# Performance work log

Measured on AMD Instinct MI355X. Metric: run time of the kernel, lower is better.

The kernel has to match this reference:

```python
import jax, jax.numpy as jnp
import numpy as np

B, N, H, E = 4, 256, 128, 32

def setup_inputs() -> dict:
    key = jax.random.key(0)
    ks = jax.random.split(key, 7)
    s = 0.05
    return {
        "node_h": jax.random.normal(ks[0], (B, N, H), dtype=jnp.float32),
        "dart_h": jax.random.normal(ks[1], (B, N, N, H), dtype=jnp.float32),
        "edge_x": jax.random.normal(ks[2], (B, N, N, E), dtype=jnp.float32),
        "W1": jax.random.normal(ks[3], (3 * H + E, H), dtype=jnp.float32) * s,
        "b1": jnp.zeros((H,), dtype=jnp.float32),
        "W2": jax.random.normal(ks[4], (H, H), dtype=jnp.float32) * s,
        "b2": jnp.zeros((H,), dtype=jnp.float32),
    }

def reference(node_h, dart_h, edge_x, W1, b1, W2, b2):
    # Split first-layer weight by concat blocks [src | dst | dart_h | edge_x]
    W1s, W1d, W1h, W1e = W1[:H], W1[H:2*H], W1[2*H:3*H], W1[3*H:]
    # Equivalent to mlp(cat([src_expand, dst_expand, dart_h, edge_x])) but
    # computes the small [B,N,H] matmuls before broadcasting to [B,N,N,H].
    pre = (jnp.einsum('bih,hk->bik', node_h, W1s)[:, :, None, :]
           + jnp.einsum('bjh,hk->bjk', node_h, W1d)[:, None, :, :]
           + jnp.einsum('bijh,hk->bijk', dart_h, W1h)
           + jnp.einsum('bije,ek->bijk', edge_x, W1e)
           + b1)
    h = jax.nn.relu(pre)
    return jnp.einsum('bijh,hk->bijk', h, W2) + b2
```

## Files before the change

kernel.cpp:

```cpp
#include <hip/hip_runtime.h>
#include <hip/hip_bf16.h>


typedef __attribute__((ext_vector_type(8))) short bf16x8;
typedef __attribute__((ext_vector_type(4))) short bf16x4;
typedef __attribute__((ext_vector_type(4))) float f32x4;

__device__ __forceinline__ unsigned short f2bf(float f) {
  union { float f; unsigned u; } v; v.f = f;
  unsigned r = v.u + 0x7FFFu + ((v.u >> 16) & 1u);
  return (unsigned short)(r >> 16);
}

__device__ __forceinline__ bf16x4 cvt4(float4 a) {
  bf16x4 r;
  r[0] = (short)f2bf(a.x); r[1] = (short)f2bf(a.y);
  r[2] = (short)f2bf(a.z); r[3] = (short)f2bf(a.w);
  return r;
}

__global__ void prep_kernel(const float* __restrict__ node, const float* __restrict__ W1,
                            const float* __restrict__ b1, const float* __restrict__ W2,
                            float* __restrict__ S, float* __restrict__ D,
                            unsigned short* __restrict__ W1hT, unsigned short* __restrict__ W1eT,
                            unsigned short* __restrict__ W2T) {
  const int t = threadIdx.x;
  if (blockIdx.x < 256) {
    __shared__ float nrow[4 * 128];
    const int bi0 = blockIdx.x * 4;
    if (t < 128)
      reinterpret_cast<float4*>(nrow)[t] = reinterpret_cast<const float4*>(node + bi0 * 128)[t];
    __syncthreads();
    const int kc = t & 127, half = t >> 7;
    float s0 = 0.f, s1 = 0.f, d0 = 0.f, d1 = 0.f;
    for (int h = 0; h < 128; ++h) {
      float ws = W1[h * 128 + kc];
      float wd = W1[(128 + h) * 128 + kc];
      float n0 = nrow[(half * 2) * 128 + h];
      float n1 = nrow[(half * 2 + 1) * 128 + h];
      s0 = fmaf(n0, ws, s0); s1 = fmaf(n1, ws, s1);
      d0 = fmaf(n0, wd, d0); d1 = fmaf(n1, wd, d1);
    }
    const float bv = b1[kc];
    S[(bi0 + half * 2) * 128 + kc] = s0 + bv;
    S[(bi0 + half * 2 + 1) * 128 + kc] = s1 + bv;
    D[(bi0 + half * 2) * 128 + kc] = d0;
    D[(bi0 + half * 2 + 1) * 128 + kc] = d1;
  } else {
    int gid = (blockIdx.x - 256) * 256 + t;
    for (int idx = gid; idx < 16384; idx += 2048)
      W1hT[idx] = f2bf(W1[(256 + (idx & 127)) * 128 + (idx >> 7)]);
    for (int idx = gid; idx < 4096; idx += 2048)
      W1eT[idx] = f2bf(W1[(384 + (idx & 31)) * 128 + (idx >> 5)]);
    for (int idx = gid; idx < 16384; idx += 2048)
      W2T[idx] = f2bf(W2[(idx & 127) * 128 + (idx >> 7)]);
  }
}

#define LDH 140
#define LDE 36

__launch_bounds__(512, 4)
__global__ void fused_kernel(const float* __restrict__ dart, const float* __restrict__ edge,
                             const float* __restrict__ S, const float* __restrict__ D,
                             const unsigned short* __restrict__ W1hT,
                             const unsigned short* __restrict__ W1eT,
                             const unsigned short* __restrict__ W2T,
                             const float* __restrict__ b2, float* __restrict__ out) {
  __shared__ unsigned short sDart[64 * LDH];
  __shared__ unsigned short sEdge[64 * LDE];
  __shared__ unsigned short sH[2][64 * LDH];

  const int tid = threadIdx.x;
  const int lane = tid & 63;
  const int wv = tid >> 6;
  const int g = lane >> 4;
  const int lj = lane & 15;

  const int bi = (blockIdx.x & 7) * 128 + (blockIdx.x >> 3);
  const int b = bi >> 8;
  const size_t m_base = (size_t)bi * 256;

  bf16x8 wh[4], we;
#pragma unroll
  for (int hs = 0; hs < 4; ++hs)
    wh[hs] = *reinterpret_cast<const bf16x8*>(&W1hT[(wv * 16 + lj) * 128 + hs * 32 + g * 8]);
  we = *reinterpret_cast<const bf16x8*>(&W1eT[(wv * 16 + lj) * 32 + g * 8]);

  float sv[4];
#pragma unroll
  for (int r = 0; r < 4; ++r)
    sv[r] = S[bi * 128 + wv * 16 + g * 4 + r];

  const int jh = wv >> 2;
  const int wn = wv & 3;
  float b2v[2][4];
#pragma unroll
  for (int nt = 0; nt < 2; ++nt)
#pragma unroll
    for (int r = 0; r < 4; ++r)
      b2v[nt][r] = b2[wn * 32 + nt * 16 + g * 4 + r];

  const int srow = tid >> 3;
  const int scol = (tid & 3 ? (tid & 7) * 4 : (tid & 7) * 4);

  for (int t = 0; t < 4; ++t) {
    const int j0 = t * 64;

    {
      const float* dsrc = dart + (m_base + j0 + srow) * 128 + scol;
      float4 rd0 = *reinterpret_cast<const float4*>(dsrc);
      float4 rd1 = *reinterpret_cast<const float4*>(dsrc + 32);
      float4 rd2 = *reinterpret_cast<const float4*>(dsrc + 64);
      float4 rd3 = *reinterpret_cast<const float4*>(dsrc + 96);
      float4 re  = *reinterpret_cast<const float4*>(edge + (m_base + j0 + srow) * 32 + scol);
      *reinterpret_cast<bf16x4*>(&sDart[srow * LDH + scol])      = cvt4(rd0);
      *reinterpret_cast<bf16x4*>(&sDart[srow * LDH + scol + 32]) = cvt4(rd1);
      *reinterpret_cast<bf16x4*>(&sDart[srow * LDH + scol + 64]) = cvt4(rd2);
      *reinterpret_cast<bf16x4*>(&sDart[srow * LDH + scol + 96]) = cvt4(rd3);
      *reinterpret_cast<bf16x4*>(&sEdge[srow * LDE + scol])      = cvt4(re);
    }
    __syncthreads();

    f32x4 dv4[4];
    {
      const float* Dp = D + (size_t)(b * 256 + j0 + lj) * 128 + wv * 16 + g * 4;
#pragma unroll
      for (int jt = 0; jt < 4; ++jt)
        dv4[jt] = *reinterpret_cast<const f32x4*>(&Dp[(size_t)(jt * 16) * 128]);
    }

    f32x4 acc1[4];
#pragma unroll
    for (int jt = 0; jt < 4; ++jt) acc1[jt] = (f32x4){0.f, 0.f, 0.f, 0.f};

#pragma unroll
    for (int hs = 0; hs < 4; ++hs) {
#pragma unroll
      for (int jt = 0; jt < 4; ++jt) {
        bf16x8 bd = *reinterpret_cast<const bf16x8*>(&sDart[(jt * 16 + lj) * LDH + hs * 32 + g * 8]);
        acc1[jt] = __builtin_amdgcn_mfma_f32_16x16x32_bf16(wh[hs], bd, acc1[jt], 0, 0, 0);
      }
    }
#pragma unroll
    for (int jt = 0; jt < 4; ++jt) {
      bf16x8 be = *reinterpret_cast<const bf16x8*>(&sEdge[(jt * 16 + lj) * LDE + g * 8]);
      acc1[jt] = __builtin_amdgcn_mfma_f32_16x16x32_bf16(we, be, acc1[jt], 0, 0, 0);
    }

    unsigned short* sHc = sH[t & 1];
#pragma unroll
    for (int jt = 0; jt < 4; ++jt) {
      bf16x4 hp;
#pragma unroll
      for (int r = 0; r < 4; ++r) {
        float x = acc1[jt][r] + sv[r] + dv4[jt][r];
        x = x > 0.f ? x : 0.f;
        hp[r] = (short)f2bf(x);
      }
      *reinterpret_cast<bf16x4*>(&sHc[(jt * 16 + lj) * LDH + wv * 16 + g * 4]) = hp;
    }
    __syncthreads();

    bf16x8 w2f[4][2];
#pragma unroll
    for (int ks = 0; ks < 4; ++ks)
#pragma unroll
      for (int nt = 0; nt < 2; ++nt)
        w2f[ks][nt] = *reinterpret_cast<const bf16x8*>(&W2T[(wn * 32 + nt * 16 + lj) * 128 + ks * 32 + g * 8]);

    f32x4 acc2[2][2];
#pragma unroll
    for (int jt = 0; jt < 2; ++jt)
#pragma unroll
      for (int nt = 0; nt < 2; ++nt) acc2[jt][nt] = (f32x4){0.f, 0.f, 0.f, 0.f};

#pragma unroll
    for (int ks = 0; ks < 4; ++ks) {
#pragma unroll
      for (int jt = 0; jt < 2; ++jt) {
        bf16x8 ah = *reinterpret_cast<const bf16x8*>(&sHc[(jh * 32 + jt * 16 + lj) * LDH + ks * 32 + g * 8]);
        acc2[jt][0] = __builtin_amdgcn_mfma_f32_16x16x32_bf16(w2f[ks][0], ah, acc2[jt][0], 0, 0, 0);
        acc2[jt][1] = __builtin_amdgcn_mfma_f32_16x16x32_bf16(w2f[ks][1], ah, acc2[jt][1], 0, 0, 0);
      }
    }

    {
      float* op = out + (m_base + j0) * 128;
#pragma unroll
      for (int jt = 0; jt < 2; ++jt)
#pragma unroll
        for (int nt = 0; nt < 2; ++nt) {
          float4 v;
          v.x = acc2[jt][nt][0] + b2v[nt][0];
          v.y = acc2[jt][nt][1] + b2v[nt][1];
          v.z = acc2[jt][nt][2] + b2v[nt][2];
          v.w = acc2[jt][nt][3] + b2v[nt][3];
          *reinterpret_cast<float4*>(&op[(size_t)(jh * 32 + jt * 16 + lj) * 128 + wn * 32 + nt * 16 + g * 4]) = v;
        }
    }
  }
}

extern "C" void kernel_launch(void* const* d_in, const int* in_sizes, int n_in,
                              void* d_out, int out_size, void* d_ws, size_t ws_size,
                              hipStream_t stream) {
  const float* node = (const float*)d_in[0];
  const float* dart = (const float*)d_in[1];
  const float* edge = (const float*)d_in[2];
  const float* W1   = (const float*)d_in[3];
  const float* b1   = (const float*)d_in[4];
  const float* W2   = (const float*)d_in[5];
  const float* b2   = (const float*)d_in[6];
  float* out = (float*)d_out;

  float* S  = (float*)d_ws;
  float* D  = S + 131072;
  unsigned short* W1hT = (unsigned short*)(D + 131072);
  unsigned short* W1eT = W1hT + 16384;
  unsigned short* W2T  = W1eT + 4096;

  hipLaunchKernelGGL(prep_kernel, dim3(264), dim3(256), 0, stream,
                     node, W1, b1, W2, S, D, W1hT, W1eT, W2T);
  hipLaunchKernelGGL(fused_kernel, dim3(1024), dim3(512), 0, stream,
                     dart, edge, S, D, W1hT, W1eT, W2T, b2, out);
}
```

Measured before the change: 98.62 us.

## Software-pipeline fused MLP: prefetch next dart tile, overlap GEMM2 with GEMM1, swizzle LDS

Restructures the fused kernel into a software pipeline. Global loads for the next 64-row dart and edge tile are issued early and written to a double-buffered LDS slot after compute, and the second GEMM for tile t-1 runs in the same iteration as the first GEMM for tile t, which cuts the barriers per tile to one. The padded LDS rows are replaced with an XOR swizzle, W2 fragments are hoisted out of the loop into registers, and the D projection is stored as bf16 to halve its reads. The cost is more registers and LDS, plus an extra bf16 rounding of D that may slightly change accuracy.

```diff
diff --git a/kernel.cpp b/kernel.cpp
--- a/kernel.cpp
+++ b/kernel.cpp
@@ -12,16 +12,33 @@
   return (unsigned short)(r >> 16);
 }
 
+__device__ __forceinline__ bf16x8 cvt8(float4 a, float4 b) {
+  bf16x8 r;
+  r[0] = (short)f2bf(a.x); r[1] = (short)f2bf(a.y);
+  r[2] = (short)f2bf(a.z); r[3] = (short)f2bf(a.w);
+  r[4] = (short)f2bf(b.x); r[5] = (short)f2bf(b.y);
+  r[6] = (short)f2bf(b.z); r[7] = (short)f2bf(b.w);
+  return r;
+}
 __device__ __forceinline__ bf16x4 cvt4(float4 a) {
   bf16x4 r;
   r[0] = (short)f2bf(a.x); r[1] = (short)f2bf(a.y);
   r[2] = (short)f2bf(a.z); r[3] = (short)f2bf(a.w);
   return r;
 }
+__device__ __forceinline__ float bf2f(short u) {
+  union { float f; unsigned v; } x;
+  x.v = ((unsigned)(unsigned short)u) << 16;
+  return x.f;
+}
+
+__device__ __forceinline__ unsigned short* swz(unsigned short* base, int row, int inrowbyte) {
+  return (unsigned short*)((char*)base + row * 256 + (inrowbyte ^ ((row & 7) << 4)));
+}
 
 __global__ void prep_kernel(const float* __restrict__ node, const float* __restrict__ W1,
                             const float* __restrict__ b1, const float* __restrict__ W2,
-                            float* __restrict__ S, float* __restrict__ D,
+                            float* __restrict__ S, unsigned short* __restrict__ Dbf,
                             unsigned short* __restrict__ W1hT, unsigned short* __restrict__ W1eT,
                             unsigned short* __restrict__ W2T) {
   const int t = threadIdx.x;
@@ -44,8 +61,8 @@
     const float bv = b1[kc];
     S[(bi0 + half * 2) * 128 + kc] = s0 + bv;
     S[(bi0 + half * 2 + 1) * 128 + kc] = s1 + bv;
-    D[(bi0 + half * 2) * 128 + kc] = d0;
-    D[(bi0 + half * 2 + 1) * 128 + kc] = d1;
+    Dbf[(size_t)(bi0 + half * 2) * 128 + kc] = f2bf(d0);
+    Dbf[(size_t)(bi0 + half * 2 + 1) * 128 + kc] = f2bf(d1);
   } else {
     int gid = (blockIdx.x - 256) * 256 + t;
     for (int idx = gid; idx < 16384; idx += 2048)
@@ -57,19 +74,18 @@
   }
 }
 
-#define LDH 140
-#define LDE 36
+#define LDE 40
 
 __launch_bounds__(512, 4)
 __global__ void fused_kernel(const float* __restrict__ dart, const float* __restrict__ edge,
-                             const float* __restrict__ S, const float* __restrict__ D,
+                             const float* __restrict__ S, const unsigned short* __restrict__ Dbf,
                              const unsigned short* __restrict__ W1hT,
                              const unsigned short* __restrict__ W1eT,
                              const unsigned short* __restrict__ W2T,
                              const float* __restrict__ b2, float* __restrict__ out) {
-  __shared__ unsigned short sDart[64 * LDH];
-  __shared__ unsigned short sEdge[64 * LDE];
-  __shared__ unsigned short sH[2][64 * LDH];
+  __shared__ unsigned short sDart[2][64 * 128];
+  __shared__ unsigned short sEdge[2][64 * LDE];
+  __shared__ unsigned short sH[2][64 * 128];
 
   const int tid = threadIdx.x;
   const int lane = tid & 63;
@@ -81,20 +97,24 @@
   const int b = bi >> 8;
   const size_t m_base = (size_t)bi * 256;
 
-  bf16x8 wh[4], we;
+  bf16x8 wh[4], we, w2f[4][2];
 #pragma unroll
   for (int hs = 0; hs < 4; ++hs)
     wh[hs] = *reinterpret_cast<const bf16x8*>(&W1hT[(wv * 16 + lj) * 128 + hs * 32 + g * 8]);
   we = *reinterpret_cast<const bf16x8*>(&W1eT[(wv * 16 + lj) * 32 + g * 8]);
 
-  float sv[4];
+  const int jh = wv >> 2;
+  const int wn = wv & 3;
+#pragma unroll
+  for (int ks = 0; ks < 4; ++ks)
+#pragma unroll
+    for (int nt = 0; nt < 2; ++nt)
+      w2f[ks][nt] = *reinterpret_cast<const bf16x8*>(&W2T[(wn * 32 + nt * 16 + lj) * 128 + ks * 32 + g * 8]);
+
+  float sv[4], b2v[2][4];
 #pragma unroll
   for (int r = 0; r < 4; ++r)
     sv[r] = S[bi * 128 + wv * 16 + g * 4 + r];
-
-  const int jh = wv >> 2;
-  const int wn = wv & 3;
-  float b2v[2][4];
 #pragma unroll
   for (int nt = 0; nt < 2; ++nt)
 #pragma unroll
@@ -102,91 +122,89 @@
       b2v[nt][r] = b2[wn * 32 + nt * 16 + g * 4 + r];
 
   const int srow = tid >> 3;
-  const int scol = (tid & 3 ? (tid & 7) * 4 : (tid & 7) * 4);
-
-  for (int t = 0; t < 4; ++t) {
-    const int j0 = t * 64;
-
-    {
-      const float* dsrc = dart + (m_base + j0 + srow) * 128 + scol;
-      float4 rd0 = *reinterpret_cast<const float4*>(dsrc);
-      float4 rd1 = *reinterpret_cast<const float4*>(dsrc + 32);
-      float4 rd2 = *reinterpret_cast<const float4*>(dsrc + 64);
-      float4 rd3 = *reinterpret_cast<const float4*>(dsrc + 96);
-      float4 re  = *reinterpret_cast<const float4*>(edge + (m_base + j0 + srow) * 32 + scol);
-      *reinterpret_cast<bf16x4*>(&sDart[srow * LDH + scol])      = cvt4(rd0);
-      *reinterpret_cast<bf16x4*>(&sDart[srow * LDH + scol + 32]) = cvt4(rd1);
-      *reinterpret_cast<bf16x4*>(&sDart[srow * LDH + scol + 64]) = cvt4(rd2);
-      *reinterpret_cast<bf16x4*>(&sDart[srow * LDH + scol + 96]) = cvt4(rd3);
-      *reinterpret_cast<bf16x4*>(&sEdge[srow * LDE + scol])      = cvt4(re);
-    }
+  const int sc = tid & 7;
+
+  {
+    const float4* p0 = reinterpret_cast<const float4*>(dart + (m_base + srow) * 128 + sc * 8);
+    const float4* p1 = reinterpret_cast<const float4*>(dart + (m_base + srow) * 128 + 64 + sc * 8);
+    float4 a0 = p0[0], a1 = p0[1], c0 = p1[0], c1 = p1[1];
+    float4 e = *reinterpret_cast<const float4*>(edge + (m_base + srow) * 32 + sc * 4);
+    *reinterpret_cast<bf16x8*>(swz(sDart[0], srow, sc * 16)) = cvt8(a0, a1);
+    *reinterpret_cast<bf16x8*>(swz(sDart[0], srow, 128 + sc * 16)) = cvt8(c0, c1);
+    *reinterpret_cast<bf16x4*>(&sEdge[0][srow * LDE + sc * 4]) = cvt4(e);
+  }
+
+  for (int t = 0; t <= 4; ++t) {
     __syncthreads();
 
-    f32x4 dv4[4];
-    {
-      const float* Dp = D + (size_t)(b * 256 + j0 + lj) * 128 + wv * 16 + g * 4;
+    float4 ra0, ra1, rc0, rc1, re;
+    if (t < 3) {
+      const size_t rbase = m_base + (size_t)(t + 1) * 64 + srow;
+      const float4* p0 = reinterpret_cast<const float4*>(dart + rbase * 128 + sc * 8);
+      const float4* p1 = reinterpret_cast<const float4*>(dart + rbase * 128 + 64 + sc * 8);
+      ra0 = p0[0]; ra1 = p0[1]; rc0 = p1[0]; rc1 = p1[1];
+      re = *reinterpret_cast<const float4*>(edge + rbase * 32 + sc * 4);
+    }
+
+    bf16x4 dvb[4];
+    if (t < 4) {
+      const unsigned short* Dp = Dbf + (size_t)(b * 256 + t * 64 + lj) * 128 + wv * 16 + g * 4;
 #pragma unroll
       for (int jt = 0; jt < 4; ++jt)
-        dv4[jt] = *reinterpret_cast<const f32x4*>(&Dp[(size_t)(jt * 16) * 128]);
-    }
-
-    f32x4 acc1[4];
-#pragma unroll
-    for (int jt = 0; jt < 4; ++jt) acc1[jt] = (f32x4){0.f, 0.f, 0.f, 0.f};
-
-#pragma unroll
-    for (int hs = 0; hs < 4; ++hs) {
+        dvb[jt] = *reinterpret_cast<const bf16x4*>(&Dp[(size_t)(jt * 16) * 128]);
+    }
+
+    if (t < 4) {
+      unsigned short* sDc = sDart[t & 1];
+      unsigned short* sEc = sEdge[t & 1];
+      f32x4 acc1[4];
+#pragma unroll
+      for (int jt = 0; jt < 4; ++jt) acc1[jt] = (f32x4){0.f, 0.f, 0.f, 0.f};
+#pragma unroll
+      for (int hs = 0; hs < 4; ++hs) {
+#pragma unroll
+        for (int jt = 0; jt < 4; ++jt) {
+          bf16x8 bd = *reinterpret_cast<const bf16x8*>(swz(sDc, jt * 16 + lj, hs * 64 + g * 16));
+          acc1[jt] = __builtin_amdgcn_mfma_f32_16x16x32_bf16(wh[hs], bd, acc1[jt], 0, 0, 0);
+        }
+      }
 #pragma unroll
       for (int jt = 0; jt < 4; ++jt) {
-        bf16x8 bd = *reinterpret_cast<const bf16x8*>(&sDart[(jt * 16 + lj) * LDH + hs * 32 + g * 8]);
-        acc1[jt] = __builtin_amdgcn_mfma_f32_16x16x32_bf16(wh[hs], bd, acc1[jt], 0, 0, 0);
-      }
-    }
-#pragma unroll
-    for (int jt = 0; jt < 4; ++jt) {
-      bf16x8 be = *reinterpret_cast<const bf16x8*>(&sEdge[(jt * 16 + lj) * LDE + g * 8]);
-      acc1[jt] = __builtin_amdgcn_mfma_f32_16x16x32_bf16(we, be, acc1[jt], 0, 0, 0);
-    }
-
-    unsigned short* sHc = sH[t & 1];
-#pragma unroll
-    for (int jt = 0; jt < 4; ++jt) {
-      bf16x4 hp;
-#pragma unroll
-      for (int r = 0; r < 4; ++r) {
-        float x = acc1[jt][r] + sv[r] + dv4[jt][r];
-        x = x > 0.f ? x : 0.f;
-        hp[r] = (short)f2bf(x);
-      }
-      *reinterpret_cast<bf16x4*>(&sHc[(jt * 16 + lj) * LDH + wv * 16 + g * 4]) = hp;
-    }
-    __syncthreads();
-
-    bf16x8 w2f[4][2];
-#pragma unroll
-    for (int ks = 0; ks < 4; ++ks)
-#pragma unroll
-      for (int nt = 0; nt < 2; ++nt)
-        w2f[ks][nt] = *reinterpret_cast<const bf16x8*>(&W2T[(wn * 32 + nt * 16 + lj) * 128 + ks * 32 + g * 8]);
-
-    f32x4 acc2[2][2];
-#pragma unroll
-    for (int jt = 0; jt < 2; ++jt)
-#pragma unroll
-      for (int nt = 0; nt < 2; ++nt) acc2[jt][nt] = (f32x4){0.f, 0.f, 0.f, 0.f};
-
-#pragma unroll
-    for (int ks = 0; ks < 4; ++ks) {
-#pragma unroll
-      for (int jt = 0; jt < 2; ++jt) {
-        bf16x8 ah = *reinterpret_cast<const bf16x8*>(&sHc[(jh * 32 + jt * 16 + lj) * LDH + ks * 32 + g * 8]);
-        acc2[jt][0] = __builtin_amdgcn_mfma_f32_16x16x32_bf16(w2f[ks][0], ah, acc2[jt][0], 0, 0, 0);
-        acc2[jt][1] = __builtin_amdgcn_mfma_f32_16x16x32_bf16(w2f[ks][1], ah, acc2[jt][1], 0, 0, 0);
-      }
-    }
-
-    {
-      float* op = out + (m_base + j0) * 128;
+        bf16x8 be = *reinterpret_cast<const bf16x8*>(&sEc[(jt * 16 + lj) * LDE + g * 8]);
+        acc1[jt] = __builtin_amdgcn_mfma_f32_16x16x32_bf16(we, be, acc1[jt], 0, 0, 0);
+      }
+
+      unsigned short* sHc = sH[t & 1];
+#pragma unroll
+      for (int jt = 0; jt < 4; ++jt) {
+        bf16x4 hp;
+#pragma unroll
+        for (int r = 0; r < 4; ++r) {
+          float x = acc1[jt][r] + sv[r] + bf2f(dvb[jt][r]);
+          x = x > 0.f ? x : 0.f;
+          hp[r] = (short)f2bf(x);
+        }
+        *reinterpret_cast<bf16x4*>(swz(sHc, jt * 16 + lj, wv * 32 + g * 8)) = hp;
+      }
+    }
+
+    if (t > 0) {
+      unsigned short* sHp = sH[(t - 1) & 1];
+      f32x4 acc2[2][2];
+#pragma unroll
+      for (int jt = 0; jt < 2; ++jt)
+#pragma unroll
+        for (int nt = 0; nt < 2; ++nt) acc2[jt][nt] = (f32x4){0.f, 0.f, 0.f, 0.f};
+#pragma unroll
+      for (int ks = 0; ks < 4; ++ks) {
+#pragma unroll
+        for (int jt = 0; jt < 2; ++jt) {
+          bf16x8 ah = *reinterpret_cast<const bf16x8*>(swz(sHp, jh * 32 + jt * 16 + lj, ks * 64 + g * 16));
+          acc2[jt][0] = __builtin_amdgcn_mfma_f32_16x16x32_bf16(w2f[ks][0], ah, acc2[jt][0], 0, 0, 0);
+          acc2[jt][1] = __builtin_amdgcn_mfma_f32_16x16x32_bf16(w2f[ks][1], ah, acc2[jt][1], 0, 0, 0);
+        }
+      }
+      float* op = out + (m_base + (size_t)(t - 1) * 64) * 128;
 #pragma unroll
       for (int jt = 0; jt < 2; ++jt)
 #pragma unroll
@@ -198,6 +216,13 @@
           v.w = acc2[jt][nt][3] + b2v[nt][3];
           *reinterpret_cast<float4*>(&op[(size_t)(jh * 32 + jt * 16 + lj) * 128 + wn * 32 + nt * 16 + g * 4]) = v;
         }
+    }
+
+    if (t < 3) {
+      unsigned short* sDn = sDart[(t + 1) & 1];
+      *reinterpret_cast<bf16x8*>(swz(sDn, srow, sc * 16)) = cvt8(ra0, ra1);
+      *reinterpret_cast<bf16x8*>(swz(sDn, srow, 128 + sc * 16)) = cvt8(rc0, rc1);
+      *reinterpret_cast<bf16x4*>(&sEdge[(t + 1) & 1][srow * LDE + sc * 4]) = cvt4(re);
     }
   }
 }
@@ -215,13 +240,13 @@
   float* out = (float*)d_out;
 
   float* S  = (float*)d_ws;
-  float* D  = S + 131072;
-  unsigned short* W1hT = (unsigned short*)(D + 131072);
+  unsigned short* Dbf  = (unsigned short*)(S + 131072);
+  unsigned short* W1hT = Dbf + 131072;
   unsigned short* W1eT = W1hT + 16384;
   unsigned short* W2T  = W1eT + 4096;
 
   hipLaunchKernelGGL(prep_kernel, dim3(264), dim3(256), 0, stream,
-                     node, W1, b1, W2, S, D, W1hT, W1eT, W2T);
+                     node, W1, b1, W2, S, Dbf, W1hT, W1eT, W2T);
   hipLaunchKernelGGL(fused_kernel, dim3(1024), dim3(512), 0, stream,
-                     dart, edge, S, D, W1hT, W1eT, W2T, b2, out);
-}
+                     dart, edge, S, Dbf, W1hT, W1eT, W2T, b2, out);
+}
```

Result: faster. 96.18 us (-2.5%).
